# Optimization experiments

Measured on AMD Instinct MI355X. Metric: run time of the kernel, lower is better.

Reference implementation:

```python
import jax, jax.numpy as jnp
import numpy as np

LN_EPS = 1e-5

def _layernorm_hd(x, gamma, beta):
    # normalize jointly over the last two axes (heads, head_dim), like nn.LayerNorm((h, d))
    mu = jnp.mean(x, axis=(-2, -1), keepdims=True)
    var = jnp.var(x, axis=(-2, -1), keepdims=True)
    return (x - mu) * jax.lax.rsqrt(var + LN_EPS) * gamma + beta

def setup_inputs() -> dict:
    key = jax.random.key(0)
    kU, kX, kq, kk, kv = jax.random.split(key, 5)
    B, N, C, H, D = 4, 8192, 256, 8, 32
    scale = (C ** 2) / H  # hidden_channels**2 / n_heads, as in the torch init
    return {
        "U": jax.random.normal(kU, (B, N, C), dtype=jnp.float32),
        "X": jax.random.uniform(kX, (B, N, 1), dtype=jnp.float32),
        "Wq": jax.random.normal(kq, (1, H, D), dtype=jnp.float32) / scale,
        "Wk": jax.random.normal(kk, (C, H, D), dtype=jnp.float32) / scale,
        "Wv": jax.random.normal(kv, (C, H, D), dtype=jnp.float32) / scale,
        "gamma": jnp.ones((H, D), dtype=jnp.float32),
        "beta": jnp.zeros((H, D), dtype=jnp.float32),
    }

def reference(U, X, Wq, Wk, Wv, gamma, beta):
    # dim_domain = 1 -> einsum command 'bnc,chd->bnhd'
    Xq = jnp.einsum('bnc,chd->bnhd', X, Wq)            # [B,N,H,D]
    Uk = jnp.einsum('bnc,chd->bnhd', U, Wk)
    Uv = jnp.einsum('bnc,chd->bnhd', U, Wv)
    # NOTE: original code applies layernorm_key to BOTH key and value (faithful reproduction)
    Uk = _layernorm_hd(Uk, gamma, beta)
    Uv = _layernorm_hd(Uv, gamma, beta)
    num_points = U.shape[1]
    kv = jnp.einsum('bnhd,bnhe->bhde', Uk, Uv)          # [B,H,D,E] small
    sa = jnp.einsum('bnhd,bhde->bneh', Xq, kv)          # [B,N,E,H]
    return (sa / num_points).reshape(U.shape)
```

## Files before the change

kernel.cpp:

```cpp
#include <hip/hip_runtime.h>
#include <math.h>

#define B_DIM 4
#define N_DIM 8192
#define C_DIM 256
#define LN_EPS 1e-5f
#define WSCALE 4096.0f
#define INV_WSCALE (1.0f/4096.0f)
#define SUM_SCALE 8192.0f
#define INV_SUM_SCALE (1.0f/8192.0f)
#define M_SCALE 67108864.0f
#define INV_M_SCALE (1.0f/67108864.0f)

typedef _Float16 f16x8 __attribute__((ext_vector_type(8)));
typedef float    f32x4 __attribute__((ext_vector_type(4)));

#define WS_WT    0
#define WS_EXT   270336
#define WS_K1    286720
#define WS_K2    286752
#define WS_PART  286976
#define WS_QK    811264

__global__ void k0a_ext(const float* __restrict__ Wq,
                        const float* __restrict__ Wk,
                        const float* __restrict__ Wv,
                        const float* __restrict__ gamma,
                        const float* __restrict__ beta,
                        char* __restrict__ ws)
{
    const int gid = blockIdx.x * 256 + threadIdx.x;
    const int k = gid >> 3;
    const int h = gid & 7;

    const float* __restrict__ wkrow = Wk + (size_t)k * C_DIM;
    const float* __restrict__ wvrow = Wv + (size_t)k * C_DIM;

    float m = 0.f, pk = 0.f, pv = 0.f;
    #pragma unroll 8
    for (int d = 0; d < 32; ++d) {
        const int c = h * 32 + d;
        const float wg = Wq[c] * gamma[c];
        const float a = wkrow[c];
        const float v = wvrow[c];
        m  = fmaf(a, wg, m);
        pk += a;
        pv += v;
    }
    #pragma unroll
    for (int msk = 1; msk <= 4; msk <<= 1) {
        pk += __shfl_xor(pk, msk, 64);
        pv += __shfl_xor(pv, msk, 64);
    }
    float* __restrict__ ext = (float*)(ws + WS_EXT);
    ext[k * 16 + h] = m * M_SCALE;
    if (h == 0) ext[k * 16 + 8] = pk * SUM_SCALE;
    if (h == 1) ext[k * 16 + 9] = pv * SUM_SCALE;
    if (h >= 2) ext[k * 16 + 8 + h] = 0.f;

    if (blockIdx.x == 0 && threadIdx.x < 8) {
        const int hh = threadIdx.x;
        float k1v = 0.f, k2v = 0.f;
        for (int d = 0; d < 32; ++d) {
            const int c = hh * 32 + d;
            k1v = fmaf(Wq[c], gamma[c], k1v);
            k2v = fmaf(Wq[c], beta[c],  k2v);
        }
        ((float*)(ws + WS_K1))[hh] = k1v;
        ((float*)(ws + WS_K2))[hh] = k2v;
    }
}

__global__ void k0b_pack(const float* __restrict__ Wk,
                         const float* __restrict__ Wv,
                         char* __restrict__ ws)
{
    __shared__ float Wl[256 * 16];
    const int t  = threadIdx.x;
    const int nt = blockIdx.x;
    const int ci = t & 15;
    const int kk = t >> 4;

    const float* __restrict__ ext = (const float*)(ws + WS_EXT);
    #pragma unroll
    for (int i = 0; i < 16; ++i) {
        const int k = i * 16 + kk;
        float v;
        if (nt < 16)      v = Wk[(size_t)k * C_DIM + nt * 16 + ci] * WSCALE;
        else if (nt < 32) v = Wv[(size_t)k * C_DIM + (nt - 16) * 16 + ci] * WSCALE;
        else              v = ext[k * 16 + ci];
        Wl[k * 16 + ci] = v;
    }
    __syncthreads();

    f16x8* __restrict__ WT = (f16x8*)(ws + WS_WT);
    const int lane = t & 63;
    const int l15  = lane & 15;
    const int hi   = lane >> 4;
    for (int kt = (t >> 6); kt < 8; kt += 4) {
        f16x8 frag;
        #pragma unroll
        for (int j = 0; j < 8; ++j)
            frag[j] = (_Float16)Wl[(kt * 32 + hi * 8 + j) * 16 + l15];
        WT[(nt * 8 + kt) * 64 + lane] = frag;
    }
}

__global__ __launch_bounds__(512, 4)
void k1_mfma_ln_reduce(const float* __restrict__ U,
                       const float* __restrict__ gamma,
                       const float* __restrict__ beta,
                       const char* __restrict__ ws_ro,
                       float* __restrict__ part)
{
    __shared__ char lds[39744];
    float*  __restrict__ T_lds = (float*)(lds + 32768);
    float*  __restrict__ sk_a  = (float*)(lds + 35072);
    float*  __restrict__ sv_a  = (float*)(lds + 35328);
    float*  __restrict__ qq    = (float*)(lds + 35584);
    float*  __restrict__ sr    = (float*)(lds + 37632);
    float2* __restrict__ DS1   = (float2*)(lds + 39680);

    const int t    = threadIdx.x;
    const int lane = t & 63;
    const int w    = t >> 6;
    const int l15  = lane & 15;
    const int rg   = lane >> 4;
    const int bid  = blockIdx.x;
    const int b    = bid >> 7;
    const int row0 = (bid & 127) * 64;

    {
        const float* __restrict__ Ub = U + ((size_t)b * N_DIM + row0) * C_DIM;
        #pragma unroll
        for (int i = 0; i < 4; ++i) {
            const int id = i * 512 + t;
            const int r  = id >> 5;
            const int kc = id & 31;
            const float4* __restrict__ src =
                (const float4*)(Ub + (size_t)r * C_DIM + kc * 8);
            const float4 v0 = src[0];
            const float4 v1 = src[1];
            f16x8 hv;
            hv[0] = (_Float16)v0.x; hv[1] = (_Float16)v0.y;
            hv[2] = (_Float16)v0.z; hv[3] = (_Float16)v0.w;
            hv[4] = (_Float16)v1.x; hv[5] = (_Float16)v1.y;
            hv[6] = (_Float16)v1.z; hv[7] = (_Float16)v1.w;
            *(f16x8*)(lds + r * 512 + ((kc * 16) ^ ((r & 7) << 4))) = hv;
        }
    }
    __syncthreads();

    f32x4 acc[4][4];
    f32x4 acce[4];
    #pragma unroll
    for (int m = 0; m < 4; ++m) {
        #pragma unroll
        for (int j = 0; j < 4; ++j) acc[m][j] = (f32x4)0.0f;
        acce[m] = (f32x4)0.0f;
    }
    {
        const f16x8* __restrict__ WT = (const f16x8*)(ws_ro + WS_WT);
        const int swz = (l15 & 7) << 4;
        const int nt0 = (w < 4) ? (w * 4) : (16 + (w - 4) * 4);
        for (int kt = 0; kt < 8; ++kt) {
            const int boff = ((kt * 64 + rg * 16) ^ swz) + l15 * 512;
            const f16x8 a0 = *(const f16x8*)(lds + boff);
            const f16x8 a1 = *(const f16x8*)(lds + boff + 8192);
            const f16x8 a2 = *(const f16x8*)(lds + boff + 16384);
            const f16x8 a3 = *(const f16x8*)(lds + boff + 24576);
            #pragma unroll
            for (int j = 0; j < 4; ++j) {
                const f16x8 bf = WT[(size_t)((nt0 + j) * 8 + kt) * 64 + lane];
                acc[0][j] = __builtin_amdgcn_mfma_f32_16x16x32_f16(a0, bf, acc[0][j], 0, 0, 0);
                acc[1][j] = __builtin_amdgcn_mfma_f32_16x16x32_f16(a1, bf, acc[1][j], 0, 0, 0);
                acc[2][j] = __builtin_amdgcn_mfma_f32_16x16x32_f16(a2, bf, acc[2][j], 0, 0, 0);
                acc[3][j] = __builtin_amdgcn_mfma_f32_16x16x32_f16(a3, bf, acc[3][j], 0, 0, 0);
            }
            if (w == 0) {
                const f16x8 bf = WT[(size_t)(32 * 8 + kt) * 64 + lane];
                acce[0] = __builtin_amdgcn_mfma_f32_16x16x32_f16(a0, bf, acce[0], 0, 0, 0);
                acce[1] = __builtin_amdgcn_mfma_f32_16x16x32_f16(a1, bf, acce[1], 0, 0, 0);
                acce[2] = __builtin_amdgcn_mfma_f32_16x16x32_f16(a2, bf, acce[2], 0, 0, 0);
                acce[3] = __builtin_amdgcn_mfma_f32_16x16x32_f16(a3, bf, acce[3], 0, 0, 0);
            }
        }
    }

    if (w == 0) {
        #pragma unroll
        for (int m = 0; m < 4; ++m)
            #pragma unroll
            for (int q = 0; q < 4; ++q) {
                const int row = m * 16 + rg * 4 + q;
                const float val = acce[m][q];
                if (l15 < 8)       T_lds[row * 9 + l15] = val * INV_M_SCALE;
                else if (l15 == 8) sk_a[row] = val * INV_SUM_SCALE;
                else if (l15 == 9) sv_a[row] = val * INV_SUM_SCALE;
            }
    }

    {
        float qp[16];
        #pragma unroll
        for (int m = 0; m < 4; ++m)
            #pragma unroll
            for (int q = 0; q < 4; ++q) {
                float s = 0.f;
                #pragma unroll
                for (int j = 0; j < 4; ++j) {
                    const float v = acc[m][j][q];
                    s = fmaf(v, v, s);
                }
                qp[m * 4 + q] = s;
            }
        #pragma unroll
        for (int i = 0; i < 16; ++i) {
            #pragma unroll
            for (int msk = 1; msk <= 8; msk <<= 1)
                qp[i] += __shfl_xor(qp[i], msk, 64);
        }
        if (l15 == 0) {
            #pragma unroll
            for (int m = 0; m < 4; ++m)
                #pragma unroll
                for (int q = 0; q < 4; ++q)
                    qq[w * 64 + m * 16 + rg * 4 + q] = qp[m * 4 + q];
        }
    }
    __syncthreads();

    if (t < 64) {
        const int r = t;
        const float sk = sk_a[r];
        const float sv = sv_a[r];
        const float qkk = (qq[0 * 64 + r] + qq[1 * 64 + r] +
                           qq[2 * 64 + r] + qq[3 * 64 + r]) * (INV_WSCALE * INV_WSCALE);
        const float qvv = (qq[4 * 64 + r] + qq[5 * 64 + r] +
                           qq[6 * 64 + r] + qq[7 * 64 + r]) * (INV_WSCALE * INV_WSCALE);
        const float muk  = sk * (1.f / 256.f);
        const float vark = qkk * (1.f / 256.f) - muk * muk;
        const float rsk  = 1.0f / sqrtf(vark + LN_EPS);
        const float muv  = sv * (1.f / 256.f);
        const float varv = qvv * (1.f / 256.f) - muv * muv;
        const float rsv  = 1.0f / sqrtf(varv + LN_EPS);
        const float wvr  = muv * rsv;
        const float* __restrict__ K1 = (const float*)(ws_ro + WS_K1);
        const float* __restrict__ K2 = (const float*)(ws_ro + WS_K2);
        #pragma unroll
        for (int h = 0; h < 8; ++h) {
            const float s = fmaf(rsk, T_lds[r * 9 + h] - muk * K1[h], K2[h]);
            sr[h * 64 + r] = s * rsv * INV_WSCALE;
            float d = s * wvr, s1 = s;
            #pragma unroll
            for (int msk = 1; msk <= 32; msk <<= 1) {
                d  += __shfl_xor(d,  msk, 64);
                s1 += __shfl_xor(s1, msk, 64);
            }
            if (r == h) DS1[h] = make_float2(d, s1);
        }
    }
    __syncthreads();

    if (w >= 4) {
        #pragma unroll
        for (int j = 0; j < 4; ++j) {
            const int h = (w - 4) * 2 + (j >> 1);
            float p = 0.f;
            #pragma unroll
            for (int m = 0; m < 4; ++m) {
                const f32x4 s4 = *(const f32x4*)&sr[h * 64 + m * 16 + rg * 4];
                p = fmaf(s4[0], acc[m][j][0], p);
                p = fmaf(s4[1], acc[m][j][1], p);
                p = fmaf(s4[2], acc[m][j][2], p);
                p = fmaf(s4[3], acc[m][j][3], p);
            }
            p += __shfl_xor(p, 16, 64);
            p += __shfl_xor(p, 32, 64);
            if (rg == 0) {
                const int c = (w - 4) * 64 + j * 16 + l15;
                const float2 ds = DS1[h];
                part[(size_t)bid * 256 + c] =
                    fmaf(gamma[c], p - ds.x, beta[c] * ds.y);
            }
        }
    }
}

__global__ void k2_reduce(const float* __restrict__ part, float* __restrict__ qk)
{
    __shared__ float red[8][32];
    const int t   = threadIdx.x;
    const int blk = blockIdx.x;
    const int b   = blk >> 3;
    const int cg  = blk & 7;
    const int c   = cg * 32 + (t & 31);
    const int seg = t >> 5;
    float s = 0.f;
    for (int i = seg * 16; i < seg * 16 + 16; ++i)
        s += part[((size_t)b * 128 + i) * 256 + c];
    red[seg][t & 31] = s;
    __syncthreads();
    if (t < 32) {
        float q = 0.f;
        #pragma unroll
        for (int sgi = 0; sgi < 8; ++sgi) q += red[sgi][t];
        qk[b * 256 + cg * 32 + t] = q;
    }
}

__global__ __launch_bounds__(256)
void k3_out(const float* __restrict__ X, const float* __restrict__ qk,
            float* __restrict__ out)
{
    __shared__ float qkp[256];
    const int t = threadIdx.x;
    const int bid = blockIdx.x;
    const int b = bid >> 8;
    const int row0 = (bid & 255) * 32;

    {
        const int h = t & 7;
        const int e = t >> 3;
        qkp[t] = qk[b * 256 + h * 32 + e] * (1.0f / (float)N_DIM);
    }
    __syncthreads();

    const int c4 = (t & 63) * 4;
    const float4 q4 = *(const float4*)&qkp[c4];
    const int rl = t >> 6;

    for (int it = 0; it < 8; ++it) {
        const int row = row0 + it * 4 + rl;
        const float x = X[(size_t)b * N_DIM + row];
        float4 o;
        o.x = x * q4.x; o.y = x * q4.y; o.z = x * q4.z; o.w = x * q4.w;
        *(float4*)&out[((size_t)b * N_DIM + row) * C_DIM + c4] = o;
    }
}

extern "C" void kernel_launch(void* const* d_in, const int* in_sizes, int n_in,
                              void* d_out, int out_size, void* d_ws, size_t ws_size,
                              hipStream_t stream)
{
    const float* U     = (const float*)d_in[0];
    const float* X     = (const float*)d_in[1];
    const float* Wq    = (const float*)d_in[2];
    const float* Wk    = (const float*)d_in[3];
    const float* Wv    = (const float*)d_in[4];
    const float* gamma = (const float*)d_in[5];
    const float* beta  = (const float*)d_in[6];
    float* out = (float*)d_out;

    char* ws = (char*)d_ws;
    float* part = (float*)(ws + WS_PART);
    float* qk   = (float*)(ws + WS_QK);

    k0a_ext<<<8, 256, 0, stream>>>(Wq, Wk, Wv, gamma, beta, ws);
    k0b_pack<<<33, 256, 0, stream>>>(Wk, Wv, ws);
    k1_mfma_ln_reduce<<<512, 512, 0, stream>>>(U, gamma, beta, ws, part);
    k2_reduce<<<32, 256, 0, stream>>>(part, qk);
    k3_out<<<1024, 256, 0, stream>>>(X, qk, out);
}
```

Before: 54.94 us.

## Halve rows per block, double-buffer weight fragments, and merge prep kernels

```diff
diff --git a/kernel.cpp b/kernel.cpp
--- a/kernel.cpp
+++ b/kernel.cpp
@@ -16,80 +16,67 @@
 typedef float    f32x4 __attribute__((ext_vector_type(4)));
 
 #define WS_WT    0
-#define WS_EXT   270336
-#define WS_K1    286720
-#define WS_K2    286752
-#define WS_PART  286976
-#define WS_QK    811264
-
-__global__ void k0a_ext(const float* __restrict__ Wq,
+#define WS_K1    270336
+#define WS_K2    270400
+#define WS_PART  270464
+#define WS_QK    1319040
+
+__global__ void k0_pack(const float* __restrict__ Wq,
                         const float* __restrict__ Wk,
                         const float* __restrict__ Wv,
                         const float* __restrict__ gamma,
                         const float* __restrict__ beta,
                         char* __restrict__ ws)
 {
-    const int gid = blockIdx.x * 256 + threadIdx.x;
-    const int k = gid >> 3;
-    const int h = gid & 7;
-
-    const float* __restrict__ wkrow = Wk + (size_t)k * C_DIM;
-    const float* __restrict__ wvrow = Wv + (size_t)k * C_DIM;
-
-    float m = 0.f, pk = 0.f, pv = 0.f;
-    #pragma unroll 8
-    for (int d = 0; d < 32; ++d) {
-        const int c = h * 32 + d;
-        const float wg = Wq[c] * gamma[c];
-        const float a = wkrow[c];
-        const float v = wvrow[c];
-        m  = fmaf(a, wg, m);
-        pk += a;
-        pv += v;
-    }
-    #pragma unroll
-    for (int msk = 1; msk <= 4; msk <<= 1) {
-        pk += __shfl_xor(pk, msk, 64);
-        pv += __shfl_xor(pv, msk, 64);
-    }
-    float* __restrict__ ext = (float*)(ws + WS_EXT);
-    ext[k * 16 + h] = m * M_SCALE;
-    if (h == 0) ext[k * 16 + 8] = pk * SUM_SCALE;
-    if (h == 1) ext[k * 16 + 9] = pv * SUM_SCALE;
-    if (h >= 2) ext[k * 16 + 8 + h] = 0.f;
-
-    if (blockIdx.x == 0 && threadIdx.x < 8) {
-        const int hh = threadIdx.x;
-        float k1v = 0.f, k2v = 0.f;
-        for (int d = 0; d < 32; ++d) {
-            const int c = hh * 32 + d;
-            k1v = fmaf(Wq[c], gamma[c], k1v);
-            k2v = fmaf(Wq[c], beta[c],  k2v);
-        }
-        ((float*)(ws + WS_K1))[hh] = k1v;
-        ((float*)(ws + WS_K2))[hh] = k2v;
-    }
-}
-
-__global__ void k0b_pack(const float* __restrict__ Wk,
-                         const float* __restrict__ Wv,
-                         char* __restrict__ ws)
-{
     __shared__ float Wl[256 * 16];
     const int t  = threadIdx.x;
     const int nt = blockIdx.x;
-    const int ci = t & 15;
-    const int kk = t >> 4;
-
-    const float* __restrict__ ext = (const float*)(ws + WS_EXT);
-    #pragma unroll
-    for (int i = 0; i < 16; ++i) {
-        const int k = i * 16 + kk;
-        float v;
-        if (nt < 16)      v = Wk[(size_t)k * C_DIM + nt * 16 + ci] * WSCALE;
-        else if (nt < 32) v = Wv[(size_t)k * C_DIM + (nt - 16) * 16 + ci] * WSCALE;
-        else              v = ext[k * 16 + ci];
-        Wl[k * 16 + ci] = v;
+
+    if (nt == 32) {
+        const int k = t;
+        const float* __restrict__ wkrow = Wk + (size_t)k * C_DIM;
+        const float* __restrict__ wvrow = Wv + (size_t)k * C_DIM;
+        float pks = 0.f, pvs = 0.f;
+        #pragma unroll
+        for (int h = 0; h < 8; ++h) {
+            float m = 0.f;
+            #pragma unroll 8
+            for (int d = 0; d < 32; ++d) {
+                const int c = h * 32 + d;
+                const float wg = Wq[c] * gamma[c];
+                const float a  = wkrow[c];
+                m = fmaf(a, wg, m);
+                pks += a;
+                pvs += wvrow[c];
+            }
+            Wl[k * 16 + h] = m * M_SCALE;
+        }
+        Wl[k * 16 + 8] = pks * SUM_SCALE;
+        Wl[k * 16 + 9] = pvs * SUM_SCALE;
+        #pragma unroll
+        for (int j = 10; j < 16; ++j) Wl[k * 16 + j] = 0.f;
+
+        if (t < 8) {
+            float k1v = 0.f, k2v = 0.f;
+            for (int d = 0; d < 32; ++d) {
+                const int c = t * 32 + d;
+                k1v = fmaf(Wq[c], gamma[c], k1v);
+                k2v = fmaf(Wq[c], beta[c],  k2v);
+            }
+            ((float*)(ws + WS_K1))[t] = k1v;
+            ((float*)(ws + WS_K2))[t] = k2v;
+        }
+    } else {
+        const int ci = t & 15;
+        const int kk = t >> 4;
+        #pragma unroll
+        for (int i = 0; i < 16; ++i) {
+            const int k = i * 16 + kk;
+            float v;
+            if (nt < 16) v = Wk[(size_t)k * C_DIM + nt * 16 + ci] * WSCALE;
+            else         v = Wv[(size_t)k * C_DIM + (nt - 16) * 16 + ci] * WSCALE;
+            Wl[k * 16 + ci] = v;
+        }
     }
     __syncthreads();
 
@@ -113,13 +100,13 @@
                        const char* __restrict__ ws_ro,
                        float* __restrict__ part)
 {
-    __shared__ char lds[39744];
-    float*  __restrict__ T_lds = (float*)(lds + 32768);
-    float*  __restrict__ sk_a  = (float*)(lds + 35072);
-    float*  __restrict__ sv_a  = (float*)(lds + 35328);
-    float*  __restrict__ qq    = (float*)(lds + 35584);
-    float*  __restrict__ sr    = (float*)(lds + 37632);
-    float2* __restrict__ DS1   = (float2*)(lds + 39680);
+    __shared__ char lds[19904];
+    float*  __restrict__ T_lds = (float*)(lds + 16384);
+    float*  __restrict__ sk_a  = (float*)(lds + 17536);
+    float*  __restrict__ sv_a  = (float*)(lds + 17664);
+    float*  __restrict__ qq    = (float*)(lds + 17792);
+    float*  __restrict__ sr    = (float*)(lds + 18816);
+    float2* __restrict__ DS1   = (float2*)(lds + 19840);
 
     const int t    = threadIdx.x;
     const int lane = t & 63;
@@ -127,13 +114,13 @@
     const int l15  = lane & 15;
     const int rg   = lane >> 4;
     const int bid  = blockIdx.x;
-    const int b    = bid >> 7;
-    const int row0 = (bid & 127) * 64;
+    const int b    = bid >> 8;
+    const int row0 = (bid & 255) * 32;
 
     {
         const float* __restrict__ Ub = U + ((size_t)b * N_DIM + row0) * C_DIM;
         #pragma unroll
-        for (int i = 0; i < 4; ++i) {
+        for (int i = 0; i < 2; ++i) {
             const int id = i * 512 + t;
             const int r  = id >> 5;
             const int kc = id & 31;
@@ -151,10 +138,10 @@
     }
     __syncthreads();
 
-    f32x4 acc[4][4];
-    f32x4 acce[4];
+    f32x4 acc[2][4];
+    f32x4 acce[2];
     #pragma unroll
-    for (int m = 0; m < 4; ++m) {
+    for (int m = 0; m < 2; ++m) {
         #pragma unroll
         for (int j = 0; j < 4; ++j) acc[m][j] = (f32x4)0.0f;
         acce[m] = (f32x4)0.0f;
@@ -163,33 +150,59 @@
         const f16x8* __restrict__ WT = (const f16x8*)(ws_ro + WS_WT);
         const int swz = (l15 & 7) << 4;
         const int nt0 = (w < 4) ? (w * 4) : (16 + (w - 4) * 4);
-        for (int kt = 0; kt < 8; ++kt) {
-            const int boff = ((kt * 64 + rg * 16) ^ swz) + l15 * 512;
-            const f16x8 a0 = *(const f16x8*)(lds + boff);
-            const f16x8 a1 = *(const f16x8*)(lds + boff + 8192);
-            const f16x8 a2 = *(const f16x8*)(lds + boff + 16384);
-            const f16x8 a3 = *(const f16x8*)(lds + boff + 24576);
-            #pragma unroll
-            for (int j = 0; j < 4; ++j) {
-                const f16x8 bf = WT[(size_t)((nt0 + j) * 8 + kt) * 64 + lane];
-                acc[0][j] = __builtin_amdgcn_mfma_f32_16x16x32_f16(a0, bf, acc[0][j], 0, 0, 0);
-                acc[1][j] = __builtin_amdgcn_mfma_f32_16x16x32_f16(a1, bf, acc[1][j], 0, 0, 0);
-                acc[2][j] = __builtin_amdgcn_mfma_f32_16x16x32_f16(a2, bf, acc[2][j], 0, 0, 0);
-                acc[3][j] = __builtin_amdgcn_mfma_f32_16x16x32_f16(a3, bf, acc[3][j], 0, 0, 0);
-            }
-            if (w == 0) {
-                const f16x8 bf = WT[(size_t)(32 * 8 + kt) * 64 + lane];
-                acce[0] = __builtin_amdgcn_mfma_f32_16x16x32_f16(a0, bf, acce[0], 0, 0, 0);
-                acce[1] = __builtin_amdgcn_mfma_f32_16x16x32_f16(a1, bf, acce[1], 0, 0, 0);
-                acce[2] = __builtin_amdgcn_mfma_f32_16x16x32_f16(a2, bf, acce[2], 0, 0, 0);
-                acce[3] = __builtin_amdgcn_mfma_f32_16x16x32_f16(a3, bf, acce[3], 0, 0, 0);
+        const int we0 = (w == 0);
+
+        f16x8 bfA[4], bfB[4], beA, beB;
+        #pragma unroll
+        for (int j = 0; j < 4; ++j) bfA[j] = WT[(size_t)((nt0 + j) * 8 + 0) * 64 + lane];
+        if (we0) beA = WT[(size_t)(32 * 8 + 0) * 64 + lane];
+
+        #pragma unroll
+        for (int kth = 0; kth < 4; ++kth) {
+            const int kt0 = kth * 2;
+            const int kt1 = kth * 2 + 1;
+            {
+                const int boff = ((kt0 * 64 + rg * 16) ^ swz) + l15 * 512;
+                const f16x8 a0 = *(const f16x8*)(lds + boff);
+                const f16x8 a1 = *(const f16x8*)(lds + boff + 8192);
+                #pragma unroll
+                for (int j = 0; j < 4; ++j) bfB[j] = WT[(size_t)((nt0 + j) * 8 + kt1) * 64 + lane];
+                if (we0) beB = WT[(size_t)(32 * 8 + kt1) * 64 + lane];
+                #pragma unroll
+                for (int j = 0; j < 4; ++j) {
+                    acc[0][j] = __builtin_amdgcn_mfma_f32_16x16x32_f16(a0, bfA[j], acc[0][j], 0, 0, 0);
+                    acc[1][j] = __builtin_amdgcn_mfma_f32_16x16x32_f16(a1, bfA[j], acc[1][j], 0, 0, 0);
+                }
+                if (we0) {
+                    acce[0] = __builtin_amdgcn_mfma_f32_16x16x32_f16(a0, beA, acce[0], 0, 0, 0);
+                    acce[1] = __builtin_amdgcn_mfma_f32_16x16x32_f16(a1, beA, acce[1], 0, 0, 0);
+                }
+            }
+            {
+                const int boff = ((kt1 * 64 + rg * 16) ^ swz) + l15 * 512;
+                const f16x8 a0 = *(const f16x8*)(lds + boff);
+                const f16x8 a1 = *(const f16x8*)(lds + boff + 8192);
+                if (kth < 3) {
+                    #pragma unroll
+                    for (int j = 0; j < 4; ++j) bfA[j] = WT[(size_t)((nt0 + j) * 8 + kt0 + 2) * 64 + lane];
+                    if (we0) beA = WT[(size_t)(32 * 8 + kt0 + 2) * 64 + lane];
+                }
+                #pragma unroll
+                for (int j = 0; j < 4; ++j) {
+                    acc[0][j] = __builtin_amdgcn_mfma_f32_16x16x32_f16(a0, bfB[j], acc[0][j], 0, 0, 0);
+                    acc[1][j] = __builtin_amdgcn_mfma_f32_16x16x32_f16(a1, bfB[j], acc[1][j], 0, 0, 0);
+                }
+                if (we0) {
+                    acce[0] = __builtin_amdgcn_mfma_f32_16x16x32_f16(a0, beB, acce[0], 0, 0, 0);
+                    acce[1] = __builtin_amdgcn_mfma_f32_16x16x32_f16(a1, beB, acce[1], 0, 0, 0);
+                }
             }
         }
     }
 
     if (w == 0) {
         #pragma unroll
-        for (int m = 0; m < 4; ++m)
+        for (int m = 0; m < 2; ++m)
             #pragma unroll
             for (int q = 0; q < 4; ++q) {
                 const int row = m * 16 + rg * 4 + q;
@@ -201,9 +214,9 @@
     }
 
     {
-        float qp[16];
-        #pragma unroll
-        for (int m = 0; m < 4; ++m)
+        float qp[8];
+        #pragma unroll
+        for (int m = 0; m < 2; ++m)
             #pragma unroll
             for (int q = 0; q < 4; ++q) {
                 float s = 0.f;
@@ -215,29 +228,29 @@
                 qp[m * 4 + q] = s;
             }
         #pragma unroll
-        for (int i = 0; i < 16; ++i) {
+        for (int i = 0; i < 8; ++i) {
             #pragma unroll
             for (int msk = 1; msk <= 8; msk <<= 1)
                 qp[i] += __shfl_xor(qp[i], msk, 64);
         }
         if (l15 == 0) {
             #pragma unroll
-            for (int m = 0; m < 4; ++m)
+            for (int m = 0; m < 2; ++m)
                 #pragma unroll
                 for (int q = 0; q < 4; ++q)
-                    qq[w * 64 + m * 16 + rg * 4 + q] = qp[m * 4 + q];
-        }
-    }
-    __syncthreads();
-
-    if (t < 64) {
+                    qq[w * 32 + m * 16 + rg * 4 + q] = qp[m * 4 + q];
+        }
+    }
+    __syncthreads();
+
+    if (t < 32) {
         const int r = t;
         const float sk = sk_a[r];
         const float sv = sv_a[r];
-        const float qkk = (qq[0 * 64 + r] + qq[1 * 64 + r] +
-                           qq[2 * 64 + r] + qq[3 * 64 + r]) * (INV_WSCALE * INV_WSCALE);
-        const float qvv = (qq[4 * 64 + r] + qq[5 * 64 + r] +
-                           qq[6 * 64 + r] + qq[7 * 64 + r]) * (INV_WSCALE * INV_WSCALE);
+        const float qkk = (qq[0 * 32 + r] + qq[1 * 32 + r] +
+                           qq[2 * 32 + r] + qq[3 * 32 + r]) * (INV_WSCALE * INV_WSCALE);
+        const float qvv = (qq[4 * 32 + r] + qq[5 * 32 + r] +
+                           qq[6 * 32 + r] + qq[7 * 32 + r]) * (INV_WSCALE * INV_WSCALE);
         const float muk  = sk * (1.f / 256.f);
         const float vark = qkk * (1.f / 256.f) - muk * muk;
         const float rsk  = 1.0f / sqrtf(vark + LN_EPS);
@@ -250,10 +263,10 @@
         #pragma unroll
         for (int h = 0; h < 8; ++h) {
             const float s = fmaf(rsk, T_lds[r * 9 + h] - muk * K1[h], K2[h]);
-            sr[h * 64 + r] = s * rsv * INV_WSCALE;
+            sr[h * 32 + r] = s * rsv * INV_WSCALE;
             float d = s * wvr, s1 = s;
             #pragma unroll
-            for (int msk = 1; msk <= 32; msk <<= 1) {
+            for (int msk = 1; msk <= 16; msk <<= 1) {
                 d  += __shfl_xor(d,  msk, 64);
                 s1 += __shfl_xor(s1, msk, 64);
             }
@@ -268,8 +281,8 @@
             const int h = (w - 4) * 2 + (j >> 1);
             float p = 0.f;
             #pragma unroll
-            for (int m = 0; m < 4; ++m) {
-                const f32x4 s4 = *(const f32x4*)&sr[h * 64 + m * 16 + rg * 4];
+            for (int m = 0; m < 2; ++m) {
+                const f32x4 s4 = *(const f32x4*)&sr[h * 32 + m * 16 + rg * 4];
                 p = fmaf(s4[0], acc[m][j][0], p);
                 p = fmaf(s4[1], acc[m][j][1], p);
                 p = fmaf(s4[2], acc[m][j][2], p);
@@ -297,8 +310,8 @@
     const int c   = cg * 32 + (t & 31);
     const int seg = t >> 5;
     float s = 0.f;
-    for (int i = seg * 16; i < seg * 16 + 16; ++i)
-        s += part[((size_t)b * 128 + i) * 256 + c];
+    for (int i = seg * 32; i < seg * 32 + 32; ++i)
+        s += part[((size_t)b * 256 + i) * 256 + c];
     red[seg][t & 31] = s;
     __syncthreads();
     if (t < 32) {
@@ -356,9 +369,8 @@
     float* part = (float*)(ws + WS_PART);
     float* qk   = (float*)(ws + WS_QK);
 
-    k0a_ext<<<8, 256, 0, stream>>>(Wq, Wk, Wv, gamma, beta, ws);
-    k0b_pack<<<33, 256, 0, stream>>>(Wk, Wv, ws);
-    k1_mfma_ln_reduce<<<512, 512, 0, stream>>>(U, gamma, beta, ws, part);
+    k0_pack<<<33, 256, 0, stream>>>(Wq, Wk, Wv, gamma, beta, ws);
+    k1_mfma_ln_reduce<<<1024, 512, 0, stream>>>(U, gamma, beta, ws, part);
     k2_reduce<<<32, 256, 0, stream>>>(part, qk);
     k3_out<<<1024, 256, 0, stream>>>(X, qk, out);
 }
```

Result: slower. 70.48 us (+28.3%).
